# Optimization experiments

Hardware: AMD Instinct MI355X
Metric: run time of the kernel (lower is better)

## Reference

```python
import jax, jax.numpy as jnp
import numpy as np

B, S, D = 4, 1024, 1024
H = 16
HD = D // H  # head_dim = 64


def setup_inputs() -> dict:
    key = jax.random.key(0)
    k1, k2, k3 = jax.random.split(key, 3)
    x = jax.random.normal(k1, (B, S, D), dtype=jnp.float32)
    # qkv_proj: Linear(input_dim, 3*embed_dim), stored as (in, out) for x @ W
    scale = 1.0 / np.sqrt(D)
    W_qkv = jax.random.uniform(k2, (D, 3 * D), dtype=jnp.float32, minval=-scale, maxval=scale)
    b_qkv = jax.random.uniform(k3, (3 * D,), dtype=jnp.float32, minval=-scale, maxval=scale)
    return {"x": x, "W_qkv": W_qkv, "b_qkv": b_qkv}


def reference(x, W_qkv, b_qkv):
    b, s, _ = x.shape
    qkv = x @ W_qkv + b_qkv                       # [B,S,3D]
    qkv = qkv.reshape(b, s, H, 3 * HD)            # [B,S,H,3*hd]
    qkv = qkv.transpose(0, 2, 1, 3)               # [B,H,S,3*hd]
    q, k, v = jnp.split(qkv, 3, axis=-1)          # each [B,H,S,hd]
    scores = jnp.einsum('bhqd,bhkd->bhqk', q, k) / jnp.sqrt(jnp.float32(HD))
    attn = jax.nn.softmax(scores, axis=-1)        # [B,H,S,S]
    out = jnp.einsum('bhqk,bhkd->bhqd', attn, v)  # [B,H,S,hd]
    values = out.transpose(0, 2, 1, 3).reshape(b, s, H * HD)  # [B,S,D]
    return values
```

## Files before the change

### kernel.cpp

```cpp
#include <hip/hip_runtime.h>
#include <hip/hip_bf16.h>
#include <stdint.h>

#define BATCH 4
#define SEQ 1024
#define DMODEL 1024
#define NH 16
#define HD 64

typedef __attribute__((ext_vector_type(8))) short short8;
typedef __attribute__((ext_vector_type(4))) float f32x4;
typedef __attribute__((ext_vector_type(4))) unsigned short ushort4v;

__device__ __forceinline__ unsigned short f2bf(float f) {
    union { float f; uint32_t u; } v; v.f = f;
    uint32_t r = v.u + 0x7fff + ((v.u >> 16) & 1);
    return (unsigned short)(r >> 16);
}

__device__ __forceinline__ uint32_t pack2bf(float lo, float hi) {
    return (uint32_t)f2bf(lo) | ((uint32_t)f2bf(hi) << 16);
}

__global__ __launch_bounds__(256) void prep_kernel(const float* __restrict__ x,
                                                   const float* __restrict__ W,
                                                   unsigned short* __restrict__ xb,
                                                   unsigned short* __restrict__ Wt) {
    __shared__ float tile[32][33];
    int bid = blockIdx.x;
    if (bid < 2048) {
        int t = bid * 256 + threadIdx.x;
        const float4* p = (const float4*)x + (size_t)t * 2;
        float4 a = p[0], b = p[1];
        short8 o;
        o[0] = (short)f2bf(a.x); o[1] = (short)f2bf(a.y);
        o[2] = (short)f2bf(a.z); o[3] = (short)f2bf(a.w);
        o[4] = (short)f2bf(b.x); o[5] = (short)f2bf(b.y);
        o[6] = (short)f2bf(b.z); o[7] = (short)f2bf(b.w);
        *((short8*)xb + t) = o;
    } else {
        int r = bid - 2048;
        int nb = (r % 96) * 32;
        int kb = (r / 96) * 32;
        int tx = threadIdx.x & 31;
        int ty = threadIdx.x >> 5;
#pragma unroll
        for (int i = 0; i < 4; i++) {
            int k = kb + ty + i * 8;
            tile[ty + i * 8][tx] = W[(size_t)k * 3072 + nb + tx];
        }
        __syncthreads();
#pragma unroll
        for (int i = 0; i < 4; i++) {
            int n = nb + ty + i * 8;
            Wt[(size_t)n * 1024 + kb + tx] = f2bf(tile[tx][ty + i * 8]);
        }
    }
}

#define BM 128
#define BN 128
#define BKK 64

__global__ __launch_bounds__(256, 3) void qkv_gemm_kernel(
    const unsigned short* __restrict__ xb,
    const unsigned short* __restrict__ wt,
    const float* __restrict__ bias,
    unsigned short* __restrict__ Qb,
    unsigned short* __restrict__ Kb,
    unsigned short* __restrict__ VbT)
{
    __shared__ __align__(16) unsigned short As[BM][64];
    __shared__ __align__(16) unsigned short Bs[BN][64];
    int tid = threadIdx.x;
    int wave = tid >> 6, lane = tid & 63;
    int quad = lane >> 4, l16 = lane & 15;
    int wm = wave >> 1, wn = wave & 1;
    int m0 = blockIdx.x * BM;
    int n0 = blockIdx.y * BN;

    int grow = lane >> 3;
    int gcol = ((lane & 7) ^ grow) << 3;
    const unsigned short* gA = xb + (size_t)(m0 + wave * 32 + grow) * 1024 + gcol;
    const unsigned short* gB = wt + (size_t)(n0 + wave * 32 + grow) * 1024 + gcol;
    unsigned short* ldsA = &As[wave * 32][0] + lane * 8;
    unsigned short* ldsB = &Bs[wave * 32][0] + lane * 8;
    int sw = l16 & 7;

    short8 areg[4], breg[4];
#pragma unroll
    for (int i = 0; i < 4; i++) {
        areg[i] = *(const short8*)(gA + (size_t)i * 8 * 1024);
        breg[i] = *(const short8*)(gB + (size_t)i * 8 * 1024);
    }

    f32x4 acc[4][4] = {};
    for (int k0 = 0; k0 < 1024; k0 += BKK) {
        __syncthreads();
#pragma unroll
        for (int i = 0; i < 4; i++) {
            *(short8*)(ldsA + i * 512) = areg[i];
            *(short8*)(ldsB + i * 512) = breg[i];
        }
        __syncthreads();
        if (k0 + BKK < 1024) {
#pragma unroll
            for (int i = 0; i < 4; i++) {
                areg[i] = *(const short8*)(gA + (size_t)i * 8 * 1024 + k0 + BKK);
                breg[i] = *(const short8*)(gB + (size_t)i * 8 * 1024 + k0 + BKK);
            }
        }
#pragma unroll
        for (int kk = 0; kk < BKK; kk += 32) {
            int kb = kk >> 3;
            short8 af[4], bf[4];
#pragma unroll
            for (int t = 0; t < 4; t++) {
                int ar = wm * 64 + t * 16 + l16;
                af[t] = *(const short8*)&As[ar][((kb + quad) ^ sw) << 3];
            }
#pragma unroll
            for (int t = 0; t < 4; t++) {
                int br = wn * 64 + t * 16 + l16;
                bf[t] = *(const short8*)&Bs[br][((kb + quad) ^ sw) << 3];
            }
#pragma unroll
            for (int mt = 0; mt < 4; mt++)
#pragma unroll
                for (int nt = 0; nt < 4; nt++)
                    acc[mt][nt] = __builtin_amdgcn_mfma_f32_16x16x32_bf16(
                        af[mt], bf[nt], acc[mt][nt], 0, 0, 0);
        }
    }
#pragma unroll
    for (int nt = 0; nt < 4; nt++) {
        int n = n0 + wn * 64 + nt * 16 + l16;
        int h = n / 192;
        int c = n - h * 192;
        int which = c >> 6;
        int d = c & 63;
        float bv = bias[n];
        if (which == 2) {
#pragma unroll
            for (int mt = 0; mt < 4; mt++) {
                int m = m0 + wm * 64 + mt * 16 + quad * 4;
                int b = m >> 10, s = m & 1023;
                ushort4v o;
                o[0] = f2bf(acc[mt][nt][0] + bv);
                o[1] = f2bf(acc[mt][nt][1] + bv);
                o[2] = f2bf(acc[mt][nt][2] + bv);
                o[3] = f2bf(acc[mt][nt][3] + bv);
                *(ushort4v*)&VbT[((size_t)((b * 16 + h) * 64 + d)) * 1024 + s] = o;
            }
        } else {
            unsigned short* dst = (which == 0) ? Qb : Kb;
            float sc = (which == 0) ? 0.125f : 1.0f;
#pragma unroll
            for (int mt = 0; mt < 4; mt++) {
#pragma unroll
                for (int r = 0; r < 4; r++) {
                    int m = m0 + wm * 64 + mt * 16 + quad * 4 + r;
                    int b = m >> 10, s = m & 1023;
                    dst[((size_t)((b * 16 + h) * 1024 + s)) * 64 + d] = f2bf((acc[mt][nt][r] + bv) * sc);
                }
            }
        }
    }
}

#define BQ 128
#define BKV 128

__global__ __launch_bounds__(256, 3) void attn_kernel(
    const unsigned short* __restrict__ Qb,
    const unsigned short* __restrict__ Kb,
    const unsigned short* __restrict__ VbT,
    float* __restrict__ out)
{
    __shared__ unsigned short Qs[BQ][64];
    __shared__ unsigned short Ks[BKV][64];
    __shared__ unsigned short Vts[HD][128];

    int tid = threadIdx.x;
    int wave = tid >> 6, lane = tid & 63;
    int quad = lane >> 4, l16 = lane & 15;

    int id = blockIdx.x;
    int xcd = id & 7, rest = id >> 3;
    int qt = rest & 7, grp = rest >> 3;
    int bh = grp * 8 + xcd;
    int q0 = qt * BQ;

    const unsigned short* Qp = Qb + (size_t)bh * SEQ * HD;
    const unsigned short* Kp = Kb + (size_t)bh * SEQ * HD;
    const unsigned short* Vp = VbT + (size_t)bh * HD * SEQ;

    int f_q = (l16 & 3) | (((l16 >> 3) & 1) << 2);
    int f_k = (l16 & 3) | (((l16 >> 2) & 1) << 2);
    int f_v = l16 & 7;
    int rbase = ((l16 >> 2) << 3) | (l16 & 3);

#pragma unroll
    for (int i = 0; i < 4; i++) {
        int idx = i * 256 + tid;
        int row = idx >> 3, pb = idx & 7;
        int fr = (row & 3) | (((row >> 3) & 1) << 2);
        int lb = pb ^ fr;
        *(short8*)&Qs[row][pb * 8] = *(const short8*)&Qp[(size_t)(q0 + row) * HD + lb * 8];
    }

    short8 kreg[4], vreg[4];
    auto load_tile = [&](int kt) {
#pragma unroll
        for (int i = 0; i < 4; i++) {
            int idx = i * 256 + tid;
            int krow = idx >> 3, kpb = idx & 7;
            int klb = kpb ^ ((krow & 3) | (((krow >> 3) & 1) << 2));
            kreg[i] = *(const short8*)&Kp[(size_t)(kt + krow) * HD + klb * 8];
            int vrow = idx >> 4, vpb = idx & 15;
            int vlb = vpb ^ (vrow & 7);
            vreg[i] = *(const short8*)&Vp[(size_t)vrow * SEQ + kt + vlb * 8];
        }
    };
    load_tile(0);

    f32x4 oacc[2][4] = {};
    float lsum[2] = {0.f, 0.f};

    for (int kt = 0; kt < SEQ; kt += BKV) {
        __syncthreads();
#pragma unroll
        for (int i = 0; i < 4; i++) {
            int idx = i * 256 + tid;
            int krow = idx >> 3, kpb = idx & 7;
            *(short8*)&Ks[krow][kpb * 8] = kreg[i];
            int vrow = idx >> 4, vpb = idx & 15;
            *(short8*)&Vts[vrow][vpb * 8] = vreg[i];
        }
        __syncthreads();
        if (kt + BKV < SEQ) load_tile(kt + BKV);

        f32x4 sacc[2][8] = {};
#pragma unroll
        for (int ds_ = 0; ds_ < HD; ds_ += 32) {
            int k0b = ds_ >> 3;
            short8 qf[2];
#pragma unroll
            for (int g = 0; g < 2; g++)
                qf[g] = *(const short8*)&Qs[wave * 32 + g * 16 + l16][((k0b + quad) ^ f_q) * 8];
#pragma unroll
            for (int nt = 0; nt < 8; nt++) {
                int krow = rbase + ((nt >> 1) << 5) + ((nt & 1) << 2);
                short8 kf = *(const short8*)&Ks[krow][((k0b + quad) ^ f_k) * 8];
#pragma unroll
                for (int g = 0; g < 2; g++)
                    sacc[g][nt] = __builtin_amdgcn_mfma_f32_16x16x32_bf16(kf, qf[g], sacc[g][nt], 0, 0, 0);
            }
        }

        uint32_t u[2][8][2];
#pragma unroll
        for (int g = 0; g < 2; g++)
#pragma unroll
            for (int nt = 0; nt < 8; nt++) {
                float p0 = __expf(sacc[g][nt][0]);
                float p1 = __expf(sacc[g][nt][1]);
                float p2 = __expf(sacc[g][nt][2]);
                float p3 = __expf(sacc[g][nt][3]);
                lsum[g] += (p0 + p1) + (p2 + p3);
                u[g][nt][0] = pack2bf(p0, p1);
                u[g][nt][1] = pack2bf(p2, p3);
            }

#pragma unroll
        for (int c = 0; c < 4; c++) {
            short8 vf[4];
#pragma unroll
            for (int nt = 0; nt < 4; nt++)
                vf[nt] = *(const short8*)&Vts[nt * 16 + l16][(((c << 2) + quad) ^ f_v) * 8];
#pragma unroll
            for (int g = 0; g < 2; g++) {
                union { uint32_t w[4]; short8 s; } pf;
                pf.w[0] = u[g][2 * c][0];
                pf.w[1] = u[g][2 * c][1];
                pf.w[2] = u[g][2 * c + 1][0];
                pf.w[3] = u[g][2 * c + 1][1];
#pragma unroll
                for (int nt = 0; nt < 4; nt++)
                    oacc[g][nt] = __builtin_amdgcn_mfma_f32_16x16x32_bf16(vf[nt], pf.s, oacc[g][nt], 0, 0, 0);
            }
        }
    }

#pragma unroll
    for (int g = 0; g < 2; g++) {
        lsum[g] += __shfl_xor(lsum[g], 16, 64);
        lsum[g] += __shfl_xor(lsum[g], 32, 64);
    }

    int b = bh >> 4, h = bh & 15;
#pragma unroll
    for (int g = 0; g < 2; g++) {
        float inv = 1.f / lsum[g];
        int s = q0 + wave * 32 + g * 16 + l16;
#pragma unroll
        for (int nt = 0; nt < 4; nt++) {
            float4 o;
            o.x = oacc[g][nt][0] * inv;
            o.y = oacc[g][nt][1] * inv;
            o.z = oacc[g][nt][2] * inv;
            o.w = oacc[g][nt][3] * inv;
            *(float4*)&out[(size_t)(b * SEQ + s) * DMODEL + h * HD + nt * 16 + quad * 4] = o;
        }
    }
}

extern "C" void kernel_launch(void* const* d_in, const int* in_sizes, int n_in,
                              void* d_out, int out_size, void* d_ws, size_t ws_size,
                              hipStream_t stream) {
    const float* x    = (const float*)d_in[0];
    const float* W    = (const float*)d_in[1];
    const float* bias = (const float*)d_in[2];
    float* out = (float*)d_out;
    char* ws = (char*)d_ws;

    unsigned short* xb  = (unsigned short*)(ws);
    unsigned short* wt  = (unsigned short*)(ws + 8388608);
    unsigned short* Qb  = (unsigned short*)(ws + 14680064);
    unsigned short* Kb  = (unsigned short*)(ws + 23068672);
    unsigned short* VbT = (unsigned short*)(ws + 31457280);

    prep_kernel<<<5120, 256, 0, stream>>>(x, W, xb, wt);
    dim3 gg(32, 24);
    qkv_gemm_kernel<<<gg, 256, 0, stream>>>(xb, wt, bias, Qb, Kb, VbT);
    attn_kernel<<<512, 256, 0, stream>>>(Qb, Kb, VbT, out);
}
```

Measured before the change: 161.2 us.

## Interleave QK score, exp and PV MFMAs per 32-key chunk in attention loop

Restructures the attention inner loop so each 32-key chunk computes its scores, exponentiates and packs them, then immediately issues the PV MFMAs, instead of computing all 128 scores first. Q fragments are loaded once per tile. This cuts live score accumulator registers (from 16 f32x4 to 4) and lets exp work overlap MFMA issue across chunks. It may lengthen dependency chains within a chunk if the compiler does not interleave chunks well.

```diff
diff --git a/kernel.cpp b/kernel.cpp
--- a/kernel.cpp
+++ b/kernel.cpp
@@ -240,51 +240,47 @@
         __syncthreads();
         if (kt + BKV < SEQ) load_tile(kt + BKV);
 
-        f32x4 sacc[2][8] = {};
-#pragma unroll
-        for (int ds_ = 0; ds_ < HD; ds_ += 32) {
-            int k0b = ds_ >> 3;
-            short8 qf[2];
+        short8 qf[2][2];
+#pragma unroll
+        for (int kc = 0; kc < 2; kc++)
 #pragma unroll
             for (int g = 0; g < 2; g++)
-                qf[g] = *(const short8*)&Qs[wave * 32 + g * 16 + l16][((k0b + quad) ^ f_q) * 8];
-#pragma unroll
-            for (int nt = 0; nt < 8; nt++) {
-                int krow = rbase + ((nt >> 1) << 5) + ((nt & 1) << 2);
-                short8 kf = *(const short8*)&Ks[krow][((k0b + quad) ^ f_k) * 8];
-#pragma unroll
-                for (int g = 0; g < 2; g++)
-                    sacc[g][nt] = __builtin_amdgcn_mfma_f32_16x16x32_bf16(kf, qf[g], sacc[g][nt], 0, 0, 0);
-            }
-        }
-
-        uint32_t u[2][8][2];
-#pragma unroll
-        for (int g = 0; g < 2; g++)
-#pragma unroll
-            for (int nt = 0; nt < 8; nt++) {
-                float p0 = __expf(sacc[g][nt][0]);
-                float p1 = __expf(sacc[g][nt][1]);
-                float p2 = __expf(sacc[g][nt][2]);
-                float p3 = __expf(sacc[g][nt][3]);
-                lsum[g] += (p0 + p1) + (p2 + p3);
-                u[g][nt][0] = pack2bf(p0, p1);
-                u[g][nt][1] = pack2bf(p2, p3);
-            }
+                qf[g][kc] = *(const short8*)&Qs[wave * 32 + g * 16 + l16][((kc * 4 + quad) ^ f_q) * 8];
 
 #pragma unroll
         for (int c = 0; c < 4; c++) {
+            int base = rbase + (c << 5);
+            f32x4 s0[2] = {}, s1[2] = {};
+#pragma unroll
+            for (int kc = 0; kc < 2; kc++) {
+                short8 kf0 = *(const short8*)&Ks[base][((kc * 4 + quad) ^ f_k) * 8];
+                short8 kf1 = *(const short8*)&Ks[base + 4][((kc * 4 + quad) ^ f_k) * 8];
+#pragma unroll
+                for (int g = 0; g < 2; g++) {
+                    s0[g] = __builtin_amdgcn_mfma_f32_16x16x32_bf16(kf0, qf[g][kc], s0[g], 0, 0, 0);
+                    s1[g] = __builtin_amdgcn_mfma_f32_16x16x32_bf16(kf1, qf[g][kc], s1[g], 0, 0, 0);
+                }
+            }
             short8 vf[4];
 #pragma unroll
             for (int nt = 0; nt < 4; nt++)
                 vf[nt] = *(const short8*)&Vts[nt * 16 + l16][(((c << 2) + quad) ^ f_v) * 8];
 #pragma unroll
             for (int g = 0; g < 2; g++) {
+                float p0 = __expf(s0[g][0]);
+                float p1 = __expf(s0[g][1]);
+                float p2 = __expf(s0[g][2]);
+                float p3 = __expf(s0[g][3]);
+                float p4 = __expf(s1[g][0]);
+                float p5 = __expf(s1[g][1]);
+                float p6 = __expf(s1[g][2]);
+                float p7 = __expf(s1[g][3]);
+                lsum[g] += ((p0 + p1) + (p2 + p3)) + ((p4 + p5) + (p6 + p7));
                 union { uint32_t w[4]; short8 s; } pf;
-                pf.w[0] = u[g][2 * c][0];
-                pf.w[1] = u[g][2 * c][1];
-                pf.w[2] = u[g][2 * c + 1][0];
-                pf.w[3] = u[g][2 * c + 1][1];
+                pf.w[0] = pack2bf(p0, p1);
+                pf.w[1] = pack2bf(p2, p3);
+                pf.w[2] = pack2bf(p4, p5);
+                pf.w[3] = pack2bf(p6, p7);
 #pragma unroll
                 for (int nt = 0; nt < 4; nt++)
                     oacc[g][nt] = __builtin_amdgcn_mfma_f32_16x16x32_bf16(vf[nt], pf.s, oacc[g][nt], 0, 0, 0);
```

Result: no change. 161.0 us (-0.1%).
